# Optimization experiments

Measured on AMD Instinct MI355X. Metric: run time of the kernel, lower is better.

Reference implementation:

```python
import jax, jax.numpy as jnp
import numpy as np

D_MODEL = 2048
N_HEADS = 16
N_KV_HEADS = 4
D_K = D_MODEL // N_HEADS  # 128
N_REP = N_HEADS // N_KV_HEADS
WINDOW = 128  # current_window_size default
RMS_EPS = 1e-8
ROPE_BASE = 10000.0
MASK_FILL = -10000.0


def _rmsnorm(x, w):
    rms = jnp.sqrt(jnp.mean(x * x, axis=-1, keepdims=True) + RMS_EPS)
    return x / rms * w


def _rope(x, cos, sin):
    # x: [B, S, H, d_k]; cos/sin: [S, d_k//2]; pairs are interleaved (..., -1, 2)
    B, S, H, dk = x.shape
    xr = x.reshape(B, S, H, dk // 2, 2)
    x1, x2 = xr[..., 0], xr[..., 1]
    c = cos[None, :, None, :]
    s = sin[None, :, None, :]
    o1 = x1 * c - x2 * s
    o2 = x1 * s + x2 * c
    return jnp.stack([o1, o2], axis=-1).reshape(B, S, H, dk)


def setup_inputs() -> dict:
    key = jax.random.key(0)
    ks = jax.random.split(key, 10)
    B, S = 2, 2048
    std = 1.0 / np.sqrt(D_MODEL)
    inp = {
        "x": jax.random.normal(ks[0], (B, S, D_MODEL), dtype=jnp.float32),
        "Wq": jax.random.normal(ks[1], (D_MODEL, D_MODEL), dtype=jnp.float32) * std,
        "bq": jnp.zeros((D_MODEL,), dtype=jnp.float32),
        "Wk": jax.random.normal(ks[2], (N_KV_HEADS * D_K, D_MODEL), dtype=jnp.float32) * std,
        "bk": jnp.zeros((N_KV_HEADS * D_K,), dtype=jnp.float32),
        "Wv": jax.random.normal(ks[3], (N_KV_HEADS * D_K, D_MODEL), dtype=jnp.float32) * std,
        "bv": jnp.zeros((N_KV_HEADS * D_K,), dtype=jnp.float32),
        "Wo": jax.random.normal(ks[4], (D_MODEL, D_MODEL), dtype=jnp.float32) * std,
        "bo": jnp.zeros((D_MODEL,), dtype=jnp.float32),
        "qn_w": jnp.ones((D_K,), dtype=jnp.float32),
        "kn_w": jnp.ones((D_K,), dtype=jnp.float32),
        "scale": jnp.asarray(1.0 / np.sqrt(D_K), dtype=jnp.float32),
    }
    return inp


def reference(x, Wq, bq, Wk, bk, Wv, bv, Wo, bo, qn_w, kn_w, scale):
    B, S, D = x.shape
    # projections
    q = (x @ Wq.T + bq).reshape(B, S, N_HEADS, D_K)
    k = (x @ Wk.T + bk).reshape(B, S, N_KV_HEADS, D_K)
    v = (x @ Wv.T + bv).reshape(B, S, N_KV_HEADS, D_K)
    # per-head RMSNorm
    q = _rmsnorm(q, qn_w)
    k = _rmsnorm(k, kn_w)
    # RoPE
    inv_freq = 1.0 / (ROPE_BASE ** (jnp.arange(0, D_K, 2, dtype=jnp.float32) / D_K))
    t = jnp.arange(S, dtype=jnp.float32)
    freqs = t[:, None] * inv_freq[None, :]  # [S, D_K//2]
    cos, sin = jnp.cos(freqs), jnp.sin(freqs)
    q = _rope(q, cos, sin)
    k = _rope(k, cos, sin)
    # [B, H, S, d_k]
    q = q.transpose(0, 2, 1, 3)
    k = k.transpose(0, 2, 1, 3)
    v = v.transpose(0, 2, 1, 3)
    # GQA repeat (repeat_interleave on head dim)
    k = jnp.repeat(k, N_REP, axis=1)
    v = jnp.repeat(v, N_REP, axis=1)
    # dense sliding-window path (window < seq_len)
    scores = jnp.einsum("bhqd,bhkd->bhqk", q, k) * scale
    idx = jnp.arange(S)
    causal = idx[:, None] < idx[None, :]  # triu diag=1
    local = jnp.abs(idx[:, None] - idx[None, :]) > (WINDOW // 2)
    mask = causal | local
    scores = jnp.where(mask[None, None, :, :], MASK_FILL, scores)
    attn = jax.nn.softmax(scores, axis=-1)
    out = jnp.einsum("bhqk,bhkd->bhqd", attn, v)
    out = out.transpose(0, 2, 1, 3).reshape(B, S, D)
    return out @ Wo.T + bo
```

## Files before the change

kernel.cpp:

```cpp
#include <hip/hip_runtime.h>

#define BATCH 2
#define SEQ 2048
#define DMODEL 2048
#define NHEADS 16
#define NKV 4
#define DK 128
#define WINH 64
#define NQKV 3072

typedef unsigned short ushort_t;
typedef __attribute__((ext_vector_type(8))) __bf16 bf16x8;
typedef __attribute__((ext_vector_type(4))) float f32x4;

__device__ __forceinline__ float b2f(ushort_t u) {
    union { unsigned int i; float f; } v; v.i = ((unsigned int)u) << 16; return v.f;
}
__device__ __forceinline__ ushort_t f2b(float f) {
    union { float f; unsigned int i; } v; v.f = f;
    unsigned int r = v.i + 0x7FFFu + ((v.i >> 16) & 1u);
    return (ushort_t)(r >> 16);
}

__device__ __forceinline__ void gload_lds16(const ushort_t* g, ushort_t* l) {
    __builtin_amdgcn_global_load_lds(
        (__attribute__((address_space(1))) void*)(void*)const_cast<ushort_t*>(g),
        (__attribute__((address_space(3))) void*)l, 16, 0, 0);
}

__global__ __launch_bounds__(256) void cvt_bf16(
    const float* __restrict__ src, ushort_t* __restrict__ dst, int n8)
{
    int i = blockIdx.x * 256 + threadIdx.x;
    if (i >= n8) return;
    float4 a = *((const float4*)src + i * 2);
    float4 b = *((const float4*)src + i * 2 + 1);
    ushort_t o[8] = { f2b(a.x), f2b(a.y), f2b(a.z), f2b(a.w),
                      f2b(b.x), f2b(b.y), f2b(b.z), f2b(b.w) };
    *((uint4*)dst + i) = *(const uint4*)o;
}

__global__ __launch_bounds__(256) void cvt_weights(
    const float* __restrict__ Wq, const float* __restrict__ Wk,
    const float* __restrict__ Wv, const float* __restrict__ Wo,
    ushort_t* __restrict__ dst)
{
    int i = blockIdx.x * 256 + threadIdx.x;
    int row = i >> 8;
    int c8  = i & 255;
    const float* src;
    if      (row < 2048) src = Wq + (size_t)row * 2048;
    else if (row < 2560) src = Wk + (size_t)(row - 2048) * 2048;
    else if (row < 3072) src = Wv + (size_t)(row - 2560) * 2048;
    else                 src = Wo + (size_t)(row - 3072) * 2048;
    float4 a = *((const float4*)src + c8 * 2);
    float4 b = *((const float4*)src + c8 * 2 + 1);
    ushort_t o[8] = { f2b(a.x), f2b(a.y), f2b(a.z), f2b(a.w),
                      f2b(b.x), f2b(b.y), f2b(b.z), f2b(b.w) };
    *((uint4*)dst + i) = *(const uint4*)o;
}

__global__ __launch_bounds__(256) void concat_bias3(
    const float* __restrict__ bq, const float* __restrict__ bk,
    const float* __restrict__ bv, float* __restrict__ dst)
{
    int i = blockIdx.x * 256 + threadIdx.x;
    if (i < 2048) dst[i] = bq[i];
    else if (i < 2560) dst[i] = bk[i - 2048];
    else if (i < 3072) dst[i] = bv[i - 2560];
}

template <typename OT>
__global__ __launch_bounds__(256) void gemm_bt(
    const ushort_t* __restrict__ A, const ushort_t* __restrict__ W,
    const float* __restrict__ bias, OT* __restrict__ C,
    int M, int N, int K)
{
    __shared__ __attribute__((aligned(16))) ushort_t sA[8192];
    __shared__ __attribute__((aligned(16))) ushort_t sB[8192];

    const int tid  = threadIdx.x;
    const int lane = tid & 63;
    const int wave = tid >> 6;
    const int nbn  = N >> 7;

    int nwg = gridDim.x;
    int bid = blockIdx.x;
    int nb  = (nwg & 7) ? bid : ((bid & 7) * (nwg >> 3) + (bid >> 3));
    const int bm = nb / nbn;
    const int bn = nb % nbn;
    const int m0 = bm << 7, n0 = bn << 7;
    const int wm = wave >> 1, wn = wave & 1;

    f32x4 acc[4][4] = {};

    const int frow = lane & 15;
    const int kg   = lane >> 4;

    const ushort_t* gA[4]; const ushort_t* gB[4];
    ushort_t* lA[4]; ushort_t* lB[4];
#pragma unroll
    for (int j = 0; j < 4; ++j) {
        int t = wave * 4 + j;
        int c = t * 64 + lane;
        int r = c >> 3, s = c & 7;
        int ksrc = s ^ (r & 7);
        gA[j] = A + (size_t)(m0 + r) * K + ksrc * 8;
        gB[j] = W + (size_t)(n0 + r) * K + ksrc * 8;
        lA[j] = sA + t * 512;
        lB[j] = sB + t * 512;
    }

    for (int k0 = 0; k0 < K; k0 += 64) {
        if (k0) __syncthreads();
#pragma unroll
        for (int j = 0; j < 4; ++j) gload_lds16(gA[j] + k0, lA[j]);
#pragma unroll
        for (int j = 0; j < 4; ++j) gload_lds16(gB[j] + k0, lB[j]);
        __syncthreads();

        bf16x8 af[4][2], bfr[4][2];
#pragma unroll
        for (int mi = 0; mi < 4; ++mi)
#pragma unroll
            for (int kk = 0; kk < 2; ++kk) {
                int r = (wm << 6) + (mi << 4) + frow;
                int sl = (kk * 4 + kg) ^ (r & 7);
                af[mi][kk] = *(const bf16x8*)(sA + (r * 8 + sl) * 8);
            }
#pragma unroll
        for (int ni = 0; ni < 4; ++ni)
#pragma unroll
            for (int kk = 0; kk < 2; ++kk) {
                int r = (wn << 6) + (ni << 4) + frow;
                int sl = (kk * 4 + kg) ^ (r & 7);
                bfr[ni][kk] = *(const bf16x8*)(sB + (r * 8 + sl) * 8);
            }
#pragma unroll
        for (int kk = 0; kk < 2; ++kk)
#pragma unroll
            for (int mi = 0; mi < 4; ++mi)
#pragma unroll
                for (int ni = 0; ni < 4; ++ni)
                    acc[mi][ni] = __builtin_amdgcn_mfma_f32_16x16x32_bf16(
                        af[mi][kk], bfr[ni][kk], acc[mi][ni], 0, 0, 0);
    }

    const int orow = (lane >> 4) << 2;
    const int ocol = lane & 15;
#pragma unroll
    for (int ni = 0; ni < 4; ++ni) {
        int col = n0 + (wn << 6) + (ni << 4) + ocol;
        float bvf = bias[col];
#pragma unroll
        for (int mi = 0; mi < 4; ++mi) {
#pragma unroll
            for (int r = 0; r < 4; ++r) {
                int row = m0 + (wm << 6) + (mi << 4) + orow + r;
                float val = acc[mi][ni][r] + bvf;
                if constexpr (sizeof(OT) == 2) C[(size_t)row * N + col] = f2b(val);
                else                           C[(size_t)row * N + col] = val;
            }
        }
    }
}

__global__ __launch_bounds__(128) void rmsrope(
    ushort_t* __restrict__ qkv, const float* __restrict__ qw,
    const float* __restrict__ kw)
{
    __shared__ float red[2];
    const int d   = threadIdx.x;
    const int blk = blockIdx.x;
    const int bs  = blk / 20;
    const int hh  = blk % 20;
    const int s   = bs & 2047;

    ushort_t* p = qkv + (size_t)bs * NQKV + hh * DK;
    const float* w = (hh < NHEADS) ? qw : kw;

    float x  = b2f(p[d]);
    float ss = x * x;
#pragma unroll
    for (int off = 32; off; off >>= 1) ss += __shfl_xor(ss, off, 64);
    if ((d & 63) == 0) red[d >> 6] = ss;
    __syncthreads();
    float tot = red[0] + red[1];
    float inv = rsqrtf(tot * (1.0f / 128.0f) + 1e-8f);
    float xn  = x * inv * w[d];

    float partner = __shfl_xor(xn, 1, 64);
    float invfreq = exp2f(-(float)(d & ~1) * (13.287712379549449f / 128.0f));
    float angle   = (float)s * invfreq;
    float c = cosf(angle), sn = sinf(angle);
    float o = (d & 1) ? (partner * sn + xn * c) : (xn * c - partner * sn);
    p[d] = f2b(o);
}

__global__ __launch_bounds__(256) void attn_mfma(
    const ushort_t* __restrict__ qkv, const float* __restrict__ scp,
    ushort_t* __restrict__ ao)
{
    __shared__ __attribute__((aligned(16))) ushort_t sK[16384];
    __shared__ __attribute__((aligned(16))) ushort_t sVT[16384];

    const int tid  = threadIdx.x;
    const int lane = tid & 63;
    const int w    = tid >> 6;
    const int c    = lane & 15;
    const int g    = lane >> 4;

    const int blk = blockIdx.x;
    const int qt  = blk & 31;
    const int h   = (blk >> 5) & 15;
    const int b   = blk >> 9;
    const int kvh = h >> 2;
    const int i0  = qt << 6;
    const int jb  = i0 - 64;
    const float scale = scp[0];

    bf16x8 aq[4];
    {
        const ushort_t* qp = qkv + ((size_t)(b * 2048 + i0 + w * 16 + c)) * NQKV
                                 + h * 128 + g * 8;
#pragma unroll
        for (int ks = 0; ks < 4; ++ks)
            aq[ks] = *(const bf16x8*)(qp + ks * 32);
    }

    const ushort_t* kvb = qkv + ((size_t)b * 2048) * NQKV + 2048 + kvh * 128;
#pragma unroll
    for (int it = 0; it < 8; ++it) {
        int idx = it * 256 + tid;
        int rr = idx >> 4, cc = idx & 15;
        int j = jb + rr; if (j < 0) j = 0;
        uint4 val = *(const uint4*)(kvb + (size_t)j * NQKV + cc * 8);
        int f2v = (rr & 15) ^ ((rr >> 3) & 15);
        *(uint4*)(sK + (rr * 16 + (cc ^ f2v)) * 8) = val;
    }
#pragma unroll
    for (int it = 0; it < 4; ++it) {
        int task = it * 256 + tid;
        int pp = task >> 4, d8 = task & 15;
        int j0 = jb + 2 * pp;     if (j0 < 0) j0 = 0;
        int j1 = jb + 2 * pp + 1; if (j1 < 0) j1 = 0;
        ushort_t e0[8]; *(uint4*)e0 = *(const uint4*)(kvb + (size_t)j0 * NQKV + 512 + d8 * 8);
        ushort_t e1[8]; *(uint4*)e1 = *(const uint4*)(kvb + (size_t)j1 * NQKV + 512 + d8 * 8);
        int cc = pp >> 2;
#pragma unroll
        for (int jj = 0; jj < 8; ++jj) {
            int rr = d8 * 8 + jj;
            int f2v = (rr & 15) ^ ((rr >> 3) & 15);
            unsigned int word = (unsigned int)e0[jj] | ((unsigned int)e1[jj] << 16);
            *(unsigned int*)(sVT + (rr * 16 + (cc ^ f2v)) * 8 + (pp & 3) * 2) = word;
        }
    }
    __syncthreads();

    f32x4 s[8] = {};
#pragma unroll
    for (int nt = 0; nt < 8; ++nt) {
        int rr = nt * 16 + c;
        int f2v = (rr & 15) ^ ((rr >> 3) & 15);
#pragma unroll
        for (int ks = 0; ks < 4; ++ks) {
            bf16x8 bk = *(const bf16x8*)(sK + (rr * 16 + ((ks * 4 + g) ^ f2v)) * 8);
            s[nt] = __builtin_amdgcn_mfma_f32_16x16x32_bf16(aq[ks], bk, s[nt], 0, 0, 0);
        }
    }

    float linv[4];
#pragma unroll
    for (int r = 0; r < 4; ++r) {
        int qb = w * 16 + g * 4 + r;
#pragma unroll
        for (int nt = 0; nt < 8; ++nt) {
            int jl = nt * 16 + c;
            bool valid = (jl >= qb) && (jl <= qb + 64) && (i0 + jl >= 64);
            s[nt][r] = valid ? s[nt][r] * scale : -1e30f;
        }
        float m = s[0][r];
#pragma unroll
        for (int nt = 1; nt < 8; ++nt) m = fmaxf(m, s[nt][r]);
#pragma unroll
        for (int off = 1; off <= 8; off <<= 1) m = fmaxf(m, __shfl_xor(m, off, 64));
        float sum = 0.f;
#pragma unroll
        for (int nt = 0; nt < 8; ++nt) {
            float e = __expf(s[nt][r] - m);
            s[nt][r] = e;
            sum += e;
        }
#pragma unroll
        for (int off = 1; off <= 8; off <<= 1) sum += __shfl_xor(sum, off, 64);
        linv[r] = 1.0f / sum;
    }

    __syncthreads();
    float* Pw = (float*)sK + w * 2048;
#pragma unroll
    for (int nt = 0; nt < 8; ++nt) {
#pragma unroll
        for (int r = 0; r < 4; ++r) {
            int q = g * 4 + r;
            int chunk = nt * 4 + (c >> 2);
            Pw[q * 128 + ((chunk ^ (q & 7)) * 4) + (c & 3)] = s[nt][r];
        }
    }

    f32x4 o[8] = {};
#pragma unroll
    for (int kt = 0; kt < 4; ++kt) {
        float pf[8];
#pragma unroll
        for (int e = 0; e < 2; ++e) {
            int chunk = kt * 8 + g * 2 + e;
            f32x4 v4 = *(const f32x4*)(Pw + c * 128 + ((chunk ^ (c & 7)) * 4));
            pf[e * 4 + 0] = v4[0]; pf[e * 4 + 1] = v4[1];
            pf[e * 4 + 2] = v4[2]; pf[e * 4 + 3] = v4[3];
        }
        ushort_t pb[8];
#pragma unroll
        for (int j = 0; j < 8; ++j) pb[j] = f2b(pf[j]);
        bf16x8 pa = *(const bf16x8*)pb;
#pragma unroll
        for (int dt = 0; dt < 8; ++dt) {
            int rr = dt * 16 + c;
            int f2v = (rr & 15) ^ ((rr >> 3) & 15);
            bf16x8 bv = *(const bf16x8*)(sVT + (rr * 16 + ((kt * 4 + g) ^ f2v)) * 8);
            o[dt] = __builtin_amdgcn_mfma_f32_16x16x32_bf16(pa, bv, o[dt], 0, 0, 0);
        }
    }

    const size_t orow0 = (size_t)(b * 2048 + i0 + w * 16);
#pragma unroll
    for (int dt = 0; dt < 8; ++dt) {
#pragma unroll
        for (int r = 0; r < 4; ++r) {
            int q = g * 4 + r;
            ao[(orow0 + q) * 2048 + h * 128 + dt * 16 + c] = f2b(o[dt][r] * linv[r]);
        }
    }
}

extern "C" void kernel_launch(void* const* d_in, const int* in_sizes, int n_in,
                              void* d_out, int out_size, void* d_ws, size_t ws_size,
                              hipStream_t stream)
{
    const float* x   = (const float*)d_in[0];
    const float* Wq  = (const float*)d_in[1];
    const float* bq  = (const float*)d_in[2];
    const float* Wk  = (const float*)d_in[3];
    const float* bk  = (const float*)d_in[4];
    const float* Wv  = (const float*)d_in[5];
    const float* bv  = (const float*)d_in[6];
    const float* Wo  = (const float*)d_in[7];
    const float* bo  = (const float*)d_in[8];
    const float* qnw = (const float*)d_in[9];
    const float* knw = (const float*)d_in[10];
    const float* scp = (const float*)d_in[11];
    float* out = (float*)d_out;

    const int M = BATCH * SEQ;
    ushort_t* xb    = (ushort_t*)d_ws;
    ushort_t* qkv0  = xb   + (size_t)M * DMODEL;
    ushort_t* Wqkvb = qkv0 + (size_t)M * NQKV;
    ushort_t* Wob   = Wqkvb + (size_t)NQKV * DMODEL;
    float*    bqkv  = (float*)(Wob + (size_t)DMODEL * DMODEL);
    ushort_t* ao    = xb;
    (void)ws_size; (void)in_sizes; (void)n_in; (void)out_size;

    cvt_bf16<<<dim3(4096), 256, 0, stream>>>(x, xb, M * DMODEL / 8);
    cvt_weights<<<dim3(5120), 256, 0, stream>>>(Wq, Wk, Wv, Wo, Wqkvb);
    concat_bias3<<<dim3(12), 256, 0, stream>>>(bq, bk, bv, bqkv);

    gemm_bt<ushort_t><<<dim3((M / 128) * (NQKV / 128)), 256, 0, stream>>>(
        xb, Wqkvb, bqkv, qkv0, M, NQKV, DMODEL);
    rmsrope<<<dim3(M * (NHEADS + NKV)), 128, 0, stream>>>(qkv0, qnw, knw);
    attn_mfma<<<dim3(BATCH * NHEADS * (SEQ / 64)), 256, 0, stream>>>(qkv0, scp, ao);
    gemm_bt<float><<<dim3((M / 128) * (DMODEL / 128)), 256, 0, stream>>>(
        ao, Wob, bo, out, M, DMODEL, DMODEL);
}
```

Baseline: 165.0 us.

## Fuse RMSNorm and RoPE into QKV GEMM epilogue; add separate output GEMM

Moves the per-head RMSNorm and RoPE into the QKV projection epilogue. A 128-column tile equals one head, so the row sum of squares is reduced with shuffles and shared memory inside the block, and the separate rmsrope kernel and its read/write pass over the QKV buffer go away. The output projection gets its own kernel with a K-step of 32, half-size LDS tiles, a different swizzle and no block remap. That new output GEMM may be less efficient than the shared template it replaces, and the fused epilogue adds an extra barrier and some register pressure.

```diff
diff --git a/kernel.cpp b/kernel.cpp
--- a/kernel.cpp
+++ b/kernel.cpp
@@ -70,14 +70,15 @@
     else if (i < 3072) dst[i] = bv[i - 2560];
 }
 
-template <typename OT>
-__global__ __launch_bounds__(256) void gemm_bt(
+__global__ __launch_bounds__(256) void gemm_qkv(
     const ushort_t* __restrict__ A, const ushort_t* __restrict__ W,
-    const float* __restrict__ bias, OT* __restrict__ C,
+    const float* __restrict__ bias, ushort_t* __restrict__ C,
+    const float* __restrict__ qn_w, const float* __restrict__ kn_w,
     int M, int N, int K)
 {
     __shared__ __attribute__((aligned(16))) ushort_t sA[8192];
     __shared__ __attribute__((aligned(16))) ushort_t sB[8192];
+    __shared__ float rbuf[2][128];
 
     const int tid  = threadIdx.x;
     const int lane = tid & 63;
@@ -148,6 +149,136 @@
 
     const int orow = (lane >> 4) << 2;
     const int ocol = lane & 15;
+
+#pragma unroll
+    for (int ni = 0; ni < 4; ++ni) {
+        float bvf = bias[n0 + (wn << 6) + (ni << 4) + ocol];
+#pragma unroll
+        for (int mi = 0; mi < 4; ++mi)
+#pragma unroll
+            for (int r = 0; r < 4; ++r)
+                acc[mi][ni][r] += bvf;
+    }
+
+    if (bn < 20) {
+        const float* w = (bn < 16) ? qn_w : kn_w;
+#pragma unroll
+        for (int mi = 0; mi < 4; ++mi)
+#pragma unroll
+            for (int r = 0; r < 4; ++r) {
+                float p = 0.f;
+#pragma unroll
+                for (int ni = 0; ni < 4; ++ni)
+                    p += acc[mi][ni][r] * acc[mi][ni][r];
+#pragma unroll
+                for (int off = 1; off <= 8; off <<= 1)
+                    p += __shfl_xor(p, off, 64);
+                if (ocol == 0)
+                    rbuf[wn][(wm << 6) + (mi << 4) + orow + r] = p;
+            }
+        __syncthreads();
+#pragma unroll
+        for (int mi = 0; mi < 4; ++mi)
+#pragma unroll
+            for (int r = 0; r < 4; ++r) {
+                int rl = (wm << 6) + (mi << 4) + orow + r;
+                float tot = rbuf[0][rl] + rbuf[1][rl];
+                float inv = rsqrtf(tot * (1.0f / 128.0f) + 1e-8f);
+                int s = (m0 + rl) & 2047;
+#pragma unroll
+                for (int ni = 0; ni < 4; ++ni) {
+                    int d = (wn << 6) + (ni << 4) + ocol;
+                    float xn = acc[mi][ni][r] * inv * w[d];
+                    float partner = __shfl_xor(xn, 1, 64);
+                    float invfreq = exp2f(-(float)(d & ~1) * (13.287712379549449f / 128.0f));
+                    float ang = (float)s * invfreq;
+                    float cs = cosf(ang), sn = sinf(ang);
+                    acc[mi][ni][r] = (d & 1) ? (partner * sn + xn * cs)
+                                             : (xn * cs - partner * sn);
+                }
+            }
+    }
+
+#pragma unroll
+    for (int ni = 0; ni < 4; ++ni) {
+        int col = n0 + (wn << 6) + (ni << 4) + ocol;
+#pragma unroll
+        for (int mi = 0; mi < 4; ++mi)
+#pragma unroll
+            for (int r = 0; r < 4; ++r) {
+                int row = m0 + (wm << 6) + (mi << 4) + orow + r;
+                C[(size_t)row * N + col] = f2b(acc[mi][ni][r]);
+            }
+    }
+}
+
+__global__ __launch_bounds__(256) void gemm_out(
+    const ushort_t* __restrict__ A, const ushort_t* __restrict__ W,
+    const float* __restrict__ bias, float* __restrict__ C,
+    int M, int N, int K)
+{
+    __shared__ __attribute__((aligned(16))) ushort_t sA[4096];
+    __shared__ __attribute__((aligned(16))) ushort_t sB[4096];
+
+    const int tid  = threadIdx.x;
+    const int lane = tid & 63;
+    const int wave = tid >> 6;
+    const int nbn  = N >> 7;
+    const int bm   = blockIdx.x / nbn;
+    const int bn   = blockIdx.x % nbn;
+    const int m0   = bm << 7, n0 = bn << 7;
+    const int wm   = wave >> 1, wn = wave & 1;
+
+    f32x4 acc[4][4] = {};
+
+    const int frow = lane & 15;
+    const int kg   = lane >> 4;
+
+    const int cc0 = wave * 2, cc1 = wave * 2 + 1;
+    const int p0 = cc0 * 64 + lane, p1 = cc1 * 64 + lane;
+    const int r0 = p0 >> 2,        r1 = p1 >> 2;
+    const int kg0 = (p0 & 3) ^ ((r0 >> 1) & 3);
+    const int kg1 = (p1 & 3) ^ ((r1 >> 1) & 3);
+    const ushort_t* gA0 = A + (size_t)(m0 + r0) * K + kg0 * 8;
+    const ushort_t* gA1 = A + (size_t)(m0 + r1) * K + kg1 * 8;
+    const ushort_t* gB0 = W + (size_t)(n0 + r0) * K + kg0 * 8;
+    const ushort_t* gB1 = W + (size_t)(n0 + r1) * K + kg1 * 8;
+    ushort_t* lA0 = sA + cc0 * 512;
+    ushort_t* lA1 = sA + cc1 * 512;
+    ushort_t* lB0 = sB + cc0 * 512;
+    ushort_t* lB1 = sB + cc1 * 512;
+
+    for (int k0 = 0; k0 < K; k0 += 32) {
+        if (k0) __syncthreads();
+        gload_lds16(gA0 + k0, lA0);
+        gload_lds16(gA1 + k0, lA1);
+        gload_lds16(gB0 + k0, lB0);
+        gload_lds16(gB1 + k0, lB1);
+        __syncthreads();
+
+        bf16x8 af[4], bfr[4];
+#pragma unroll
+        for (int mi = 0; mi < 4; ++mi) {
+            int r = (wm << 6) + (mi << 4) + frow;
+            int slot = kg ^ ((r >> 1) & 3);
+            af[mi] = *(const bf16x8*)(sA + (((r << 2) | slot) << 3));
+        }
+#pragma unroll
+        for (int ni = 0; ni < 4; ++ni) {
+            int r = (wn << 6) + (ni << 4) + frow;
+            int slot = kg ^ ((r >> 1) & 3);
+            bfr[ni] = *(const bf16x8*)(sB + (((r << 2) | slot) << 3));
+        }
+#pragma unroll
+        for (int mi = 0; mi < 4; ++mi)
+#pragma unroll
+            for (int ni = 0; ni < 4; ++ni)
+                acc[mi][ni] = __builtin_amdgcn_mfma_f32_16x16x32_bf16(
+                    af[mi], bfr[ni], acc[mi][ni], 0, 0, 0);
+    }
+
+    const int orow = (lane >> 4) << 2;
+    const int ocol = lane & 15;
 #pragma unroll
     for (int ni = 0; ni < 4; ++ni) {
         int col = n0 + (wn << 6) + (ni << 4) + ocol;
@@ -157,44 +288,10 @@
 #pragma unroll
             for (int r = 0; r < 4; ++r) {
                 int row = m0 + (wm << 6) + (mi << 4) + orow + r;
-                float val = acc[mi][ni][r] + bvf;
-                if constexpr (sizeof(OT) == 2) C[(size_t)row * N + col] = f2b(val);
-                else                           C[(size_t)row * N + col] = val;
-            }
-        }
-    }
-}
-
-__global__ __launch_bounds__(128) void rmsrope(
-    ushort_t* __restrict__ qkv, const float* __restrict__ qw,
-    const float* __restrict__ kw)
-{
-    __shared__ float red[2];
-    const int d   = threadIdx.x;
-    const int blk = blockIdx.x;
-    const int bs  = blk / 20;
-    const int hh  = blk % 20;
-    const int s   = bs & 2047;
-
-    ushort_t* p = qkv + (size_t)bs * NQKV + hh * DK;
-    const float* w = (hh < NHEADS) ? qw : kw;
-
-    float x  = b2f(p[d]);
-    float ss = x * x;
-#pragma unroll
-    for (int off = 32; off; off >>= 1) ss += __shfl_xor(ss, off, 64);
-    if ((d & 63) == 0) red[d >> 6] = ss;
-    __syncthreads();
-    float tot = red[0] + red[1];
-    float inv = rsqrtf(tot * (1.0f / 128.0f) + 1e-8f);
-    float xn  = x * inv * w[d];
-
-    float partner = __shfl_xor(xn, 1, 64);
-    float invfreq = exp2f(-(float)(d & ~1) * (13.287712379549449f / 128.0f));
-    float angle   = (float)s * invfreq;
-    float c = cosf(angle), sn = sinf(angle);
-    float o = (d & 1) ? (partner * sn + xn * c) : (xn * c - partner * sn);
-    p[d] = f2b(o);
+                C[(size_t)row * N + col] = acc[mi][ni][r] + bvf;
+            }
+        }
+    }
 }
 
 __global__ __launch_bounds__(256) void attn_mfma(
@@ -374,10 +471,9 @@
     cvt_weights<<<dim3(5120), 256, 0, stream>>>(Wq, Wk, Wv, Wo, Wqkvb);
     concat_bias3<<<dim3(12), 256, 0, stream>>>(bq, bk, bv, bqkv);
 
-    gemm_bt<ushort_t><<<dim3((M / 128) * (NQKV / 128)), 256, 0, stream>>>(
-        xb, Wqkvb, bqkv, qkv0, M, NQKV, DMODEL);
-    rmsrope<<<dim3(M * (NHEADS + NKV)), 128, 0, stream>>>(qkv0, qnw, knw);
+    gemm_qkv<<<dim3((M / 128) * (NQKV / 128)), 256, 0, stream>>>(
+        xb, Wqkvb, bqkv, qkv0, qnw, knw, M, NQKV, DMODEL);
     attn_mfma<<<dim3(BATCH * NHEADS * (SEQ / 64)), 256, 0, stream>>>(qkv0, scp, ao);
-    gemm_bt<float><<<dim3((M / 128) * (DMODEL / 128)), 256, 0, stream>>>(
+    gemm_out<<<dim3((M / 128) * (DMODEL / 128)), 256, 0, stream>>>(
         ao, Wob, bo, out, M, DMODEL, DMODEL);
 }
```

After: 541.9 us. 228% more time.

## Split output projection K-loop across two wave groups with LDS reduction

Applied to the files above, without the earlier changes.

Replaces the templated GEMM for the output projection with a 512-thread kernel. Two groups of four waves each handle half of every 64-wide K slice, and their partial accumulators are summed through shared memory before the bias is added and fp32 written out. The aim is more waves per tile, so latency is better hidden on the 256-block output GEMM, which underfills the GPU. The cost is a larger LDS footprint (64KB) and an extra reduction pass. The rmsrope change adds only an unused shuffle.

```diff
diff --git a/kernel.cpp b/kernel.cpp
--- a/kernel.cpp
+++ b/kernel.cpp
@@ -70,10 +70,9 @@
     else if (i < 3072) dst[i] = bv[i - 2560];
 }
 
-template <typename OT>
-__global__ __launch_bounds__(256) void gemm_bt(
+__global__ __launch_bounds__(256) void gemm_qkv(
     const ushort_t* __restrict__ A, const ushort_t* __restrict__ W,
-    const float* __restrict__ bias, OT* __restrict__ C,
+    const float* __restrict__ bias, ushort_t* __restrict__ C,
     int M, int N, int K)
 {
     __shared__ __attribute__((aligned(16))) ushort_t sA[8192];
@@ -157,9 +156,7 @@
 #pragma unroll
             for (int r = 0; r < 4; ++r) {
                 int row = m0 + (wm << 6) + (mi << 4) + orow + r;
-                float val = acc[mi][ni][r] + bvf;
-                if constexpr (sizeof(OT) == 2) C[(size_t)row * N + col] = f2b(val);
-                else                           C[(size_t)row * N + col] = val;
+                C[(size_t)row * N + col] = f2b(acc[mi][ni][r] + bvf);
             }
         }
     }
@@ -169,7 +166,6 @@
     ushort_t* __restrict__ qkv, const float* __restrict__ qw,
     const float* __restrict__ kw)
 {
-    __shared__ float red[2];
     const int d   = threadIdx.x;
     const int blk = blockIdx.x;
     const int bs  = blk / 20;
@@ -183,9 +179,12 @@
     float ss = x * x;
 #pragma unroll
     for (int off = 32; off; off >>= 1) ss += __shfl_xor(ss, off, 64);
+    float s2 = __shfl_xor(ss, 0, 64);
+    __shared__ float red[2];
     if ((d & 63) == 0) red[d >> 6] = ss;
     __syncthreads();
     float tot = red[0] + red[1];
+    (void)s2;
     float inv = rsqrtf(tot * (1.0f / 128.0f) + 1e-8f);
     float xn  = x * inv * w[d];
 
@@ -195,6 +194,110 @@
     float c = cosf(angle), sn = sinf(angle);
     float o = (d & 1) ? (partner * sn + xn * c) : (xn * c - partner * sn);
     p[d] = f2b(o);
+}
+
+__global__ __launch_bounds__(512) void gemm_out_ks(
+    const ushort_t* __restrict__ A, const ushort_t* __restrict__ W,
+    const float* __restrict__ bias, float* __restrict__ C,
+    int M, int N, int K)
+{
+    __shared__ __attribute__((aligned(16))) unsigned char smem[65536];
+    ushort_t* sA = (ushort_t*)smem;
+    ushort_t* sB = (ushort_t*)(smem + 16384);
+    float*    red = (float*)smem;
+
+    const int tid  = threadIdx.x;
+    const int lane = tid & 63;
+    const int wave = tid >> 6;
+    const int g    = wave >> 2;
+    const int q    = wave & 3;
+    const int wm   = q >> 1, wn = q & 1;
+    const int nbn  = N >> 7;
+
+    int nwg = gridDim.x;
+    int bid = blockIdx.x;
+    int nb  = (nwg & 7) ? bid : ((bid & 7) * (nwg >> 3) + (bid >> 3));
+    const int bm = nb / nbn;
+    const int bn = nb % nbn;
+    const int m0 = bm << 7, n0 = bn << 7;
+
+    f32x4 acc[4][4] = {};
+
+    const int frow = lane & 15;
+    const int kg   = lane >> 4;
+
+    const ushort_t* gA[2]; const ushort_t* gB[2];
+    ushort_t* lA[2]; ushort_t* lB[2];
+#pragma unroll
+    for (int j = 0; j < 2; ++j) {
+        int t = wave * 2 + j;
+        int c = t * 64 + lane;
+        int r = c >> 3, s = c & 7;
+        int ksrc = s ^ (r & 7);
+        gA[j] = A + (size_t)(m0 + r) * K + ksrc * 8;
+        gB[j] = W + (size_t)(n0 + r) * K + ksrc * 8;
+        lA[j] = sA + t * 512;
+        lB[j] = sB + t * 512;
+    }
+
+    for (int k0 = 0; k0 < K; k0 += 64) {
+        if (k0) __syncthreads();
+#pragma unroll
+        for (int j = 0; j < 2; ++j) gload_lds16(gA[j] + k0, lA[j]);
+#pragma unroll
+        for (int j = 0; j < 2; ++j) gload_lds16(gB[j] + k0, lB[j]);
+        __syncthreads();
+
+        bf16x8 af[4], bfr[4];
+#pragma unroll
+        for (int mi = 0; mi < 4; ++mi) {
+            int r = (wm << 6) + (mi << 4) + frow;
+            int sl = ((g << 2) + kg) ^ (r & 7);
+            af[mi] = *(const bf16x8*)(sA + (r * 8 + sl) * 8);
+        }
+#pragma unroll
+        for (int ni = 0; ni < 4; ++ni) {
+            int r = (wn << 6) + (ni << 4) + frow;
+            int sl = ((g << 2) + kg) ^ (r & 7);
+            bfr[ni] = *(const bf16x8*)(sB + (r * 8 + sl) * 8);
+        }
+#pragma unroll
+        for (int mi = 0; mi < 4; ++mi)
+#pragma unroll
+            for (int ni = 0; ni < 4; ++ni)
+                acc[mi][ni] = __builtin_amdgcn_mfma_f32_16x16x32_bf16(
+                    af[mi], bfr[ni], acc[mi][ni], 0, 0, 0);
+    }
+
+    __syncthreads();
+    if (g == 1) {
+#pragma unroll
+        for (int mi = 0; mi < 4; ++mi)
+#pragma unroll
+            for (int ni = 0; ni < 4; ++ni)
+                *(f32x4*)(red + q * 4096 + (mi * 4 + ni) * 256 + lane * 4) =
+                    acc[mi][ni];
+    }
+    __syncthreads();
+
+    if (g == 0) {
+        const int orow = (lane >> 4) << 2;
+        const int ocol = lane & 15;
+#pragma unroll
+        for (int ni = 0; ni < 4; ++ni) {
+            int col = n0 + (wn << 6) + (ni << 4) + ocol;
+            float bvf = bias[col];
+#pragma unroll
+            for (int mi = 0; mi < 4; ++mi) {
+                f32x4 other = *(const f32x4*)(red + q * 4096 + (mi * 4 + ni) * 256 + lane * 4);
+#pragma unroll
+                for (int r = 0; r < 4; ++r) {
+                    int row = m0 + (wm << 6) + (mi << 4) + orow + r;
+                    C[(size_t)row * N + col] = acc[mi][ni][r] + other[r] + bvf;
+                }
+            }
+        }
+    }
 }
 
 __global__ __launch_bounds__(256) void attn_mfma(
@@ -374,10 +477,10 @@
     cvt_weights<<<dim3(5120), 256, 0, stream>>>(Wq, Wk, Wv, Wo, Wqkvb);
     concat_bias3<<<dim3(12), 256, 0, stream>>>(bq, bk, bv, bqkv);
 
-    gemm_bt<ushort_t><<<dim3((M / 128) * (NQKV / 128)), 256, 0, stream>>>(
+    gemm_qkv<<<dim3((M / 128) * (NQKV / 128)), 256, 0, stream>>>(
         xb, Wqkvb, bqkv, qkv0, M, NQKV, DMODEL);
     rmsrope<<<dim3(M * (NHEADS + NKV)), 128, 0, stream>>>(qkv0, qnw, knw);
     attn_mfma<<<dim3(BATCH * NHEADS * (SEQ / 64)), 256, 0, stream>>>(qkv0, scp, ao);
-    gemm_bt<float><<<dim3((M / 128) * (DMODEL / 128)), 256, 0, stream>>>(
+    gemm_out_ks<<<dim3((M / 128) * (DMODEL / 128)), 512, 0, stream>>>(
         ao, Wob, bo, out, M, DMODEL, DMODEL);
 }
```

New measurement: 164.5 us. About the same (-0.3%).
